# Kernel optimization log

Measured on AMD Instinct MI355X. Metric: run time of the kernel, lower is better.

The kernel has to match this reference:

```python
import jax, jax.numpy as jnp
import numpy as np
import math

PI = math.pi
PHI = (1.0 + math.sqrt(5.0)) / 2.0
D_MODEL = 1024
N_HEADS = 16
D_HEAD = D_MODEL // N_HEADS
LAYER_DEPTH = 0.5
LAYER_INDEX = 0
CONV_RATE = 0.1


def setup_inputs() -> dict:
    key = jax.random.key(0)
    ks = jax.random.split(key, 5)
    B, T = 2, 2048
    x = jax.random.normal(ks[0], (B, T, D_MODEL), dtype=jnp.float32)
    s = 1.0 / math.sqrt(D_MODEL)
    Wq = jax.random.normal(ks[1], (D_MODEL, D_MODEL), dtype=jnp.float32) * s
    Wk = jax.random.normal(ks[2], (D_MODEL, D_MODEL), dtype=jnp.float32) * s
    Wv = jax.random.normal(ks[3], (D_MODEL, D_MODEL), dtype=jnp.float32) * s
    We = jax.random.normal(ks[4], (D_MODEL, D_MODEL), dtype=jnp.float32) * s
    # per-head chamber init, matching ApertureChamber / _head_depth
    frac = jnp.arange(N_HEADS, dtype=jnp.float32) / max(N_HEADS - 1, 1)
    lo = LAYER_DEPTH * 0.5
    hi = 0.5 + LAYER_DEPTH * 0.5
    depth = lo + frac * (hi - lo)
    beta = 0.5 + 0.2 * (1.0 - 2.0 * depth)           # [H] raw (pre-sigmoid) params
    input_valve = jnp.full((N_HEADS,), 0.5, dtype=jnp.float32)
    output_valve = jnp.full((N_HEADS,), 0.5, dtype=jnp.float32)
    chi = jnp.ones((N_HEADS,), dtype=jnp.float32)
    return {"x": x, "Wq": Wq, "Wk": Wk, "Wv": Wv, "We": We,
            "beta": beta, "input_valve": input_valve,
            "output_valve": output_valve, "chi": chi}


def reference(x, Wq, Wk, Wv, We, beta, input_valve, output_valve, chi):
    B, T, D = x.shape
    H, dh = N_HEADS, D // N_HEADS
    conv_factor = 1.0 / PHI ** (LAYER_INDEX * CONV_RATE)
    scale = math.sqrt(dh * conv_factor)
    # QKV projections (torch Linear: x @ W.T), split heads -> [B,H,T,dh]
    q = (x @ Wq.T).reshape(B, T, H, dh).transpose(0, 2, 1, 3)
    k = (x @ Wk.T).reshape(B, T, H, dh).transpose(0, 2, 1, 3)
    v = (x @ Wv.T).reshape(B, T, H, dh).transpose(0, 2, 1, 3)
    attn = jax.nn.softmax(jnp.einsum('bhqd,bhkd->bhqk', q, k) / scale, axis=-1)
    converged = jnp.einsum('bhqk,bhkd->bhqd', attn, v)  # [B,H,T,dh]
    # ApertureChamber per head, vectorized over H (broadcast [H] -> [1,H,1,1])
    b = jax.nn.sigmoid(beta)[None, :, None, None]
    iv = jax.nn.sigmoid(input_valve)[None, :, None, None]
    ov = jax.nn.sigmoid(output_valve)[None, :, None, None]
    g = jnp.tanh(chi)[None, :, None, None]
    ang = PI * b
    ca, sa = jnp.cos(ang), jnp.sin(ang)
    x_in = converged * iv
    half = dh // 2  # d_head even -> no leftover lane
    xr, xi = x_in[..., :half], x_in[..., half:]
    rot = jnp.concatenate([xr * ca - xi * sa, xr * sa + xi * ca], axis=-1)
    out = rot * ov * g  # output valve + tanh(chi) gate
    combined = out.transpose(0, 2, 1, 3).reshape(B, T, D)
    return combined @ We.T
```

## Files before the change

kernel.cpp:

```cpp
#include <hip/hip_runtime.h>
#include <hip/hip_bf16.h>
#include <math.h>

typedef __bf16 bf16;
typedef __bf16 bf16x4 __attribute__((ext_vector_type(4)));
typedef __bf16 bf16x8 __attribute__((ext_vector_type(8)));
typedef float f32x4 __attribute__((ext_vector_type(4)));
typedef float f32x16 __attribute__((ext_vector_type(16)));
typedef unsigned int u32x4 __attribute__((ext_vector_type(4)));

static __device__ __forceinline__ f32x4 mfma16(bf16x8 a, bf16x8 b, f32x4 c) {
  return __builtin_amdgcn_mfma_f32_16x16x32_bf16(a, b, c, 0, 0, 0);
}
static __device__ __forceinline__ f32x16 mfma32(bf16x8 a, bf16x8 b, f32x16 c) {
  return __builtin_amdgcn_mfma_f32_32x32x16_bf16(a, b, c, 0, 0, 0);
}
static __device__ __forceinline__ void gld_lds16(const void* g, void* l) {
  __builtin_amdgcn_global_load_lds(
      (const __attribute__((address_space(1))) void*)g,
      (__attribute__((address_space(3))) void*)l, 16, 0, 0);
}
static __device__ __forceinline__ unsigned cvt_pk_bf16(float lo, float hi) {
  unsigned r;
  asm("v_cvt_pk_bf16_f32 %0, %1, %2" : "=v"(r) : "v"(lo), "v"(hi));
  return r;
}
static __device__ __forceinline__ float rsum16(f32x16 v) {
  float a0 = v[0] + v[8],  a1 = v[1] + v[9];
  float a2 = v[2] + v[10], a3 = v[3] + v[11];
  float a4 = v[4] + v[12], a5 = v[5] + v[13];
  float a6 = v[6] + v[14], a7 = v[7] + v[15];
  a0 += a4; a1 += a5; a2 += a6; a3 += a7;
  return (a0 + a1) + (a2 + a3);
}

__global__ void cast_all(const float* __restrict__ x, const float* __restrict__ Wq,
                         const float* __restrict__ Wk, const float* __restrict__ Wv,
                         const float* __restrict__ We,
                         bf16* __restrict__ xb, bf16* __restrict__ qb,
                         bf16* __restrict__ kb, bf16* __restrict__ vb,
                         bf16* __restrict__ eb) {
  int i = blockIdx.x * 256 + threadIdx.x;
  const float* s; bf16* d; int off;
  if (i < 1048576) { s = x; d = xb; off = i; }
  else {
    int j = i - 1048576; int w = j >> 18; off = j & 262143;
    s = (w == 0) ? Wq : (w == 1) ? Wk : (w == 2) ? Wv : We;
    d = (w == 0) ? qb : (w == 1) ? kb : (w == 2) ? vb : eb;
  }
  float4 v = reinterpret_cast<const float4*>(s)[off];
  bf16x4 o; o[0] = (bf16)v.x; o[1] = (bf16)v.y; o[2] = (bf16)v.z; o[3] = (bf16)v.w;
  reinterpret_cast<bf16x4*>(d)[off] = o;
}

template<int MODE>
__global__ void gemm_bt(const bf16* __restrict__ A,
                        const bf16* __restrict__ B0, const bf16* __restrict__ B1,
                        const bf16* __restrict__ B2,
                        void* __restrict__ C0v, void* __restrict__ C1v, void* __restrict__ C2v,
                        int M, int N, int K) {
  __shared__ bf16 As[128 * 64];
  __shared__ bf16 Bs[128 * 64];
  const int tid = threadIdx.x;
  const int wave = tid >> 6;
  const int lane = tid & 63;
  const int bid = blockIdx.x | (blockIdx.y << 3) | (blockIdx.z << 8);
  const int cpx = gridDim.z << 5;
  const int swz = (bid & 7) * cpx + (bid >> 3);
  const int n0 = (swz & 7) * 128;
  const int m0 = ((swz >> 3) & 31) * 128;
  const int zz = swz >> 8;
  const bf16* B = (zz == 0) ? B0 : (zz == 1) ? B1 : B2;
  void* Cv = (zz == 0) ? C0v : (zz == 1) ? C1v : C2v;
  const int wr = (wave >> 1) * 64;
  const int wc = (wave & 1) * 64;
  const int frow = lane & 15;
  const int fx = frow & 7;
  const int khi = lane >> 4;
  const int srow8 = lane >> 3;
  const int scol = ((lane & 7) ^ srow8) * 8;
  f32x4 acc[4][4] = {};
  char* AsB = (char*)As;
  char* BsB = (char*)Bs;
  for (int k0 = 0; k0 < K; k0 += 64) {
    __syncthreads();
#pragma unroll
    for (int j = 0; j < 4; ++j) {
      int u = j * 4 + wave;
      int row = u * 8 + srow8;
      gld_lds16(&A[(size_t)(m0 + row) * K + k0 + scol], AsB + u * 1024);
      gld_lds16(&B[(size_t)(n0 + row) * K + k0 + scol], BsB + u * 1024);
    }
    asm volatile("s_waitcnt vmcnt(0)" ::: "memory");
    __syncthreads();
#pragma unroll
    for (int kk = 0; kk < 2; ++kk) {
      bf16x8 af[4], bfr[4];
#pragma unroll
      for (int mi = 0; mi < 4; ++mi)
        af[mi] = *reinterpret_cast<const bf16x8*>(
            AsB + (wr + mi * 16 + frow) * 128 + (((kk << 2) + khi) ^ fx) * 16);
#pragma unroll
      for (int ni = 0; ni < 4; ++ni)
        bfr[ni] = *reinterpret_cast<const bf16x8*>(
            BsB + (wc + ni * 16 + frow) * 128 + (((kk << 2) + khi) ^ fx) * 16);
      __builtin_amdgcn_s_setprio(1);
#pragma unroll
      for (int mi = 0; mi < 4; ++mi)
#pragma unroll
        for (int ni = 0; ni < 4; ++ni)
          acc[mi][ni] = mfma16(af[mi], bfr[ni], acc[mi][ni]);
      __builtin_amdgcn_s_setprio(0);
    }
  }
#pragma unroll
  for (int mi = 0; mi < 4; ++mi) {
#pragma unroll
    for (int ni = 0; ni < 4; ++ni) {
#pragma unroll
      for (int r = 0; r < 4; ++r) {
        int row = m0 + wr + mi * 16 + khi * 4 + r;
        int col = n0 + wc + ni * 16 + frow;
        if (MODE == 0) {
          int b = row >> 11, t = row & 2047, h = col >> 6, d = col & 63;
          ((bf16*)Cv)[(((size_t)b * 16 + h) * 2048 + t) * 64 + d] = (bf16)acc[mi][ni][r];
        } else {
          ((float*)Cv)[(size_t)row * N + col] = acc[mi][ni][r];
        }
      }
    }
  }
}

__global__ void transpose_v(const bf16* __restrict__ v, bf16* __restrict__ vt) {
  __shared__ bf16 tile[64][65];
  int bh = blockIdx.y;
  int t0 = blockIdx.x * 64;
  for (int idx = threadIdx.x; idx < 64 * 64; idx += 256) {
    int r = idx >> 6, c = idx & 63;
    tile[r][c] = v[((size_t)bh * 2048 + t0 + r) * 64 + c];
  }
  __syncthreads();
  for (int idx = threadIdx.x; idx < 64 * 64; idx += 256) {
    int d = idx >> 6, r = idx & 63;
    vt[((size_t)bh * 64 + d) * 2048 + t0 + r] = tile[r][d];
  }
}

__global__ __launch_bounds__(256, 4)
void attn_kernel(const bf16* __restrict__ q, const bf16* __restrict__ k,
                 const bf16* __restrict__ vt,
                 const float* __restrict__ beta, const float* __restrict__ ivp,
                 const float* __restrict__ ovp, const float* __restrict__ chip,
                 bf16* __restrict__ comb) {
  __shared__ bf16 Ks[2][64 * 64];
  __shared__ bf16 Vs[2][64 * 64];
  const int tid = threadIdx.x;
  const int wave = tid >> 6, lane = tid & 63;
  const int hi = lane >> 5, ln = lane & 31;
  const int bid = blockIdx.x | (blockIdx.y << 4);
  const int swz = (bid & 7) * 64 + (bid >> 3);
  const int qblk = swz & 15, bh = swz >> 4;
  const int h = bh & 15, b = bh >> 4;
  const int q0w = qblk * 128 + wave * 32;
  const float C = 0.18033688011112042f;
  const float SHIFT = 28.853900817779268f;

  const bf16* qrow = q + ((size_t)bh * 2048 + q0w + ln) * 64 + hi * 8;
  bf16x8 qf[4];
#pragma unroll
  for (int ds = 0; ds < 4; ++ds)
    qf[ds] = *reinterpret_cast<const bf16x8*>(qrow + ds * 16);

  const bf16* kbase = k + (size_t)bh * 2048 * 64;
  const bf16* vbase = vt + (size_t)bh * 64 * 2048;
  const int srow = lane >> 3;
  const int scol = ((lane & 7) ^ (srow & 7)) * 8;

  f32x16 acc0 = {}, acc1 = {}, ps = {};

  auto stage = [&](int buf, int k0) {
#pragma unroll
    for (int j = 0; j < 2; ++j) {
      int u = wave * 2 + j;
      int r = u * 8 + srow;
      gld_lds16(&kbase[(size_t)(k0 + r) * 64 + scol], (char*)&Ks[buf][0] + u * 1024);
      gld_lds16(&vbase[(size_t)r * 2048 + k0 + scol], (char*)&Vs[buf][0] + u * 1024);
    }
  };

  stage(0, 0);
  int cur = 0;
  for (int k0 = 0; k0 < 2048; k0 += 64) {
    asm volatile("s_waitcnt vmcnt(0)" ::: "memory");
    __syncthreads();
    if (k0 + 64 < 2048) stage(cur ^ 1, k0 + 64);

    f32x16 s[2];
    s[0] = (f32x16){}; s[1] = (f32x16){};
    const char* kb = (const char*)&Ks[cur][0];
    __builtin_amdgcn_s_setprio(1);
#pragma unroll
    for (int kh = 0; kh < 2; ++kh) {
      const int r = kh * 32 + ln;
      const int rx = (r & 7) << 4;
#pragma unroll
      for (int ds = 0; ds < 4; ++ds) {
        bf16x8 kf = *reinterpret_cast<const bf16x8*>(kb + r * 128 + ((ds * 32 + hi * 16) ^ rx));
        s[kh] = mfma32(kf, qf[ds], s[kh]);
      }
    }
    __builtin_amdgcn_s_setprio(0);

#pragma unroll
    for (int kh = 0; kh < 2; ++kh) {
      f32x16 z = s[kh] * C - SHIFT;
#pragma unroll
      for (int e = 0; e < 16; ++e) s[kh][e] = exp2f(z[e]);
      ps += s[kh];
    }

    const char* vb = (const char*)&Vs[cur][0];
#pragma unroll
    for (int ks = 0; ks < 4; ++ks) {
      const int kh = ks >> 1;
      const int b0 = 8 * (ks & 1);
      unsigned a0 = cvt_pk_bf16(s[kh][b0 + 0], s[kh][b0 + 1]);
      unsigned a1 = cvt_pk_bf16(s[kh][b0 + 4], s[kh][b0 + 5]);
      unsigned c0 = cvt_pk_bf16(s[kh][b0 + 2], s[kh][b0 + 3]);
      unsigned c1 = cvt_pk_bf16(s[kh][b0 + 6], s[kh][b0 + 7]);
      asm("v_permlane32_swap_b32 %0, %1" : "+v"(a0), "+v"(a1));
      asm("v_permlane32_swap_b32 %0, %1" : "+v"(c0), "+v"(c1));
      union { u32x4 u; bf16x8 v; } pf;
      pf.u[0] = a0; pf.u[1] = c0; pf.u[2] = a1; pf.u[3] = c1;
      __builtin_amdgcn_s_setprio(1);
#pragma unroll
      for (int dh = 0; dh < 2; ++dh) {
        const int r = dh * 32 + ln;
        bf16x8 vf = *reinterpret_cast<const bf16x8*>(
            vb + r * 128 + ((ks * 32 + hi * 16) ^ ((r & 7) << 4)));
        if (dh == 0) acc0 = mfma32(pf.v, vf, acc0);
        else         acc1 = mfma32(pf.v, vf, acc1);
      }
      __builtin_amdgcn_s_setprio(0);
    }
    cur ^= 1;
  }

  float lsum = rsum16(ps);
  lsum += __shfl_xor(lsum, 32);
  float inv = 1.f / lsum;

  float bb = 1.f / (1.f + expf(-beta[h]));
  float ang = 3.14159265358979323846f * bb;
  float ca = cosf(ang), sa = sinf(ang);
  float iv = 1.f / (1.f + expf(-ivp[h]));
  float ov = 1.f / (1.f + expf(-ovp[h]));
  float g = tanhf(chip[h]);
  float K1 = iv * ov * g * ca;
  float K2 = iv * ov * g * sa;
#pragma unroll
  for (int r = 0; r < 16; ++r) {
    int qr = (r & 3) + 8 * (r >> 2) + 4 * hi;
    float iq = __shfl(inv, qr, 32);
    float o_r = acc0[r] * iq, o_i = acc1[r] * iq;
    size_t base = ((size_t)b * 2048 + q0w + qr) * 1024 + (size_t)h * 64;
    comb[base + ln]      = (bf16)(K1 * o_r - K2 * o_i);
    comb[base + 32 + ln] = (bf16)(K2 * o_r + K1 * o_i);
  }
}

extern "C" void kernel_launch(void* const* d_in, const int* in_sizes, int n_in,
                              void* d_out, int out_size, void* d_ws, size_t ws_size,
                              hipStream_t stream) {
  const float* x    = (const float*)d_in[0];
  const float* Wq   = (const float*)d_in[1];
  const float* Wk   = (const float*)d_in[2];
  const float* Wv   = (const float*)d_in[3];
  const float* We   = (const float*)d_in[4];
  const float* beta = (const float*)d_in[5];
  const float* ivp  = (const float*)d_in[6];
  const float* ovp  = (const float*)d_in[7];
  const float* chip = (const float*)d_in[8];

  char* ws = (char*)d_ws;
  bf16* x_bf  = (bf16*)(ws + (size_t)0);
  bf16* Wq_bf = (bf16*)(ws + ((size_t)8  << 20));
  bf16* Wk_bf = (bf16*)(ws + ((size_t)10 << 20));
  bf16* Wv_bf = (bf16*)(ws + ((size_t)12 << 20));
  bf16* We_bf = (bf16*)(ws + ((size_t)14 << 20));
  bf16* q_bf  = (bf16*)(ws + ((size_t)16 << 20));
  bf16* k_bf  = (bf16*)(ws + ((size_t)24 << 20));
  bf16* v_bf  = (bf16*)(ws + ((size_t)32 << 20));
  bf16* v_t   = (bf16*)(ws + ((size_t)40 << 20));
  bf16* comb  = (bf16*)(ws + ((size_t)48 << 20));

  cast_all<<<8192, 256, 0, stream>>>(x, Wq, Wk, Wv, We, x_bf, Wq_bf, Wk_bf, Wv_bf, We_bf);

  gemm_bt<0><<<dim3(8, 32, 3), 256, 0, stream>>>(x_bf, Wq_bf, Wk_bf, Wv_bf,
                                                 q_bf, k_bf, v_bf, 4096, 1024, 1024);
  transpose_v<<<dim3(32, 32), 256, 0, stream>>>(v_bf, v_t);
  attn_kernel<<<dim3(16, 32), 256, 0, stream>>>(q_bf, k_bf, v_t, beta, ivp, ovp, chip, comb);
  gemm_bt<1><<<dim3(8, 32, 1), 256, 0, stream>>>(comb, We_bf, We_bf, We_bf,
                                                 d_out, d_out, d_out, 4096, 1024, 1024);
}
```

Baseline: 226.8 us.

## Split attention KV range across two wave groups and merge partial sums in LDS

Doubles the attention block to 512 threads, where two groups of four waves each process half of the key/value sequence for the same 128 queries, with separate double-buffered LDS tiles. After the loop, group 1 writes its unnormalized accumulators and row sums to LDS and group 0 adds them before normalizing and applying the rotation gate. The goal is more waves in flight per query tile to hide latency and shorten the per-block serial loop. The cost is double the LDS per block (64KB), a cross-group reduction through shared memory, and possibly lower occupancy. The fixed softmax shift keeps the merge a plain sum.

```diff
diff --git a/kernel.cpp b/kernel.cpp
--- a/kernel.cpp
+++ b/kernel.cpp
@@ -147,22 +147,23 @@
   }
 }
 
-__global__ __launch_bounds__(256, 4)
+__global__ __launch_bounds__(512, 4)
 void attn_kernel(const bf16* __restrict__ q, const bf16* __restrict__ k,
                  const bf16* __restrict__ vt,
                  const float* __restrict__ beta, const float* __restrict__ ivp,
                  const float* __restrict__ ovp, const float* __restrict__ chip,
                  bf16* __restrict__ comb) {
-  __shared__ bf16 Ks[2][64 * 64];
-  __shared__ bf16 Vs[2][64 * 64];
+  __shared__ bf16 Ks[2][2][64 * 64];
+  __shared__ bf16 Vs[2][2][64 * 64];
   const int tid = threadIdx.x;
   const int wave = tid >> 6, lane = tid & 63;
+  const int w4 = wave & 3, grp = wave >> 2;
   const int hi = lane >> 5, ln = lane & 31;
   const int bid = blockIdx.x | (blockIdx.y << 4);
   const int swz = (bid & 7) * 64 + (bid >> 3);
   const int qblk = swz & 15, bh = swz >> 4;
   const int h = bh & 15, b = bh >> 4;
-  const int q0w = qblk * 128 + wave * 32;
+  const int q0w = qblk * 128 + w4 * 32;
   const float C = 0.18033688011112042f;
   const float SHIFT = 28.853900817779268f;
 
@@ -172,33 +173,34 @@
   for (int ds = 0; ds < 4; ++ds)
     qf[ds] = *reinterpret_cast<const bf16x8*>(qrow + ds * 16);
 
-  const bf16* kbase = k + (size_t)bh * 2048 * 64;
-  const bf16* vbase = vt + (size_t)bh * 64 * 2048;
+  const bf16* kbase = k + (size_t)bh * 2048 * 64 + (size_t)grp * 1024 * 64;
+  const bf16* vbase = vt + (size_t)bh * 64 * 2048 + grp * 1024;
   const int srow = lane >> 3;
   const int scol = ((lane & 7) ^ (srow & 7)) * 8;
 
-  f32x16 acc0 = {}, acc1 = {}, ps = {};
+  f32x16 acc0 = {}, acc1 = {};
+  float lsum = 0.f;
 
   auto stage = [&](int buf, int k0) {
 #pragma unroll
     for (int j = 0; j < 2; ++j) {
-      int u = wave * 2 + j;
+      int u = w4 * 2 + j;
       int r = u * 8 + srow;
-      gld_lds16(&kbase[(size_t)(k0 + r) * 64 + scol], (char*)&Ks[buf][0] + u * 1024);
-      gld_lds16(&vbase[(size_t)r * 2048 + k0 + scol], (char*)&Vs[buf][0] + u * 1024);
+      gld_lds16(&kbase[(size_t)(k0 + r) * 64 + scol], (char*)&Ks[grp][buf][0] + u * 1024);
+      gld_lds16(&vbase[(size_t)r * 2048 + k0 + scol], (char*)&Vs[grp][buf][0] + u * 1024);
     }
   };
 
   stage(0, 0);
   int cur = 0;
-  for (int k0 = 0; k0 < 2048; k0 += 64) {
+  for (int k0 = 0; k0 < 1024; k0 += 64) {
     asm volatile("s_waitcnt vmcnt(0)" ::: "memory");
     __syncthreads();
-    if (k0 + 64 < 2048) stage(cur ^ 1, k0 + 64);
+    if (k0 + 64 < 1024) stage(cur ^ 1, k0 + 64);
 
     f32x16 s[2];
     s[0] = (f32x16){}; s[1] = (f32x16){};
-    const char* kb = (const char*)&Ks[cur][0];
+    const char* kb = (const char*)&Ks[grp][cur][0];
     __builtin_amdgcn_s_setprio(1);
 #pragma unroll
     for (int kh = 0; kh < 2; ++kh) {
@@ -217,10 +219,10 @@
       f32x16 z = s[kh] * C - SHIFT;
 #pragma unroll
       for (int e = 0; e < 16; ++e) s[kh][e] = exp2f(z[e]);
-      ps += s[kh];
-    }
-
-    const char* vb = (const char*)&Vs[cur][0];
+      lsum += rsum16(s[kh]);
+    }
+
+    const char* vb = (const char*)&Vs[grp][cur][0];
 #pragma unroll
     for (int ks = 0; ks < 4; ++ks) {
       const int kh = ks >> 1;
@@ -247,26 +249,46 @@
     cur ^= 1;
   }
 
-  float lsum = rsum16(ps);
-  lsum += __shfl_xor(lsum, 32);
-  float inv = 1.f / lsum;
-
-  float bb = 1.f / (1.f + expf(-beta[h]));
-  float ang = 3.14159265358979323846f * bb;
-  float ca = cosf(ang), sa = sinf(ang);
-  float iv = 1.f / (1.f + expf(-ivp[h]));
-  float ov = 1.f / (1.f + expf(-ovp[h]));
-  float g = tanhf(chip[h]);
-  float K1 = iv * ov * g * ca;
-  float K2 = iv * ov * g * sa;
-#pragma unroll
-  for (int r = 0; r < 16; ++r) {
-    int qr = (r & 3) + 8 * (r >> 2) + 4 * hi;
-    float iq = __shfl(inv, qr, 32);
-    float o_r = acc0[r] * iq, o_i = acc1[r] * iq;
-    size_t base = ((size_t)b * 2048 + q0w + qr) * 1024 + (size_t)h * 64;
-    comb[base + ln]      = (bf16)(K1 * o_r - K2 * o_i);
-    comb[base + 32 + ln] = (bf16)(K2 * o_r + K1 * o_i);
+  __syncthreads();
+  float* exO = (float*)&Ks[0][0][0];
+  float* exL = (float*)&Vs[0][0][0];
+  const int xl = w4 * 64 + lane;
+  if (grp == 1) {
+#pragma unroll
+    for (int r = 0; r < 16; ++r) {
+      exO[r * 256 + xl]        = acc0[r];
+      exO[(16 + r) * 256 + xl] = acc1[r];
+    }
+    exL[xl] = lsum;
+  }
+  __syncthreads();
+  if (grp == 0) {
+#pragma unroll
+    for (int r = 0; r < 16; ++r) {
+      acc0[r] += exO[r * 256 + xl];
+      acc1[r] += exO[(16 + r) * 256 + xl];
+    }
+    lsum += exL[xl];
+    lsum += __shfl_xor(lsum, 32);
+    float inv = 1.f / lsum;
+
+    float bb = 1.f / (1.f + expf(-beta[h]));
+    float ang = 3.14159265358979323846f * bb;
+    float ca = cosf(ang), sa = sinf(ang);
+    float iv = 1.f / (1.f + expf(-ivp[h]));
+    float ov = 1.f / (1.f + expf(-ovp[h]));
+    float g = tanhf(chip[h]);
+    float K1 = iv * ov * g * ca;
+    float K2 = iv * ov * g * sa;
+#pragma unroll
+    for (int r = 0; r < 16; ++r) {
+      int qr = (r & 3) + 8 * (r >> 2) + 4 * hi;
+      float iq = __shfl(inv, qr, 32);
+      float o_r = acc0[r] * iq, o_i = acc1[r] * iq;
+      size_t base = ((size_t)b * 2048 + q0w + qr) * 1024 + (size_t)h * 64;
+      comb[base + ln]      = (bf16)(K1 * o_r - K2 * o_i);
+      comb[base + 32 + ln] = (bf16)(K2 * o_r + K1 * o_i);
+    }
   }
 }
 
@@ -300,7 +322,7 @@
   gemm_bt<0><<<dim3(8, 32, 3), 256, 0, stream>>>(x_bf, Wq_bf, Wk_bf, Wv_bf,
                                                  q_bf, k_bf, v_bf, 4096, 1024, 1024);
   transpose_v<<<dim3(32, 32), 256, 0, stream>>>(v_bf, v_t);
-  attn_kernel<<<dim3(16, 32), 256, 0, stream>>>(q_bf, k_bf, v_t, beta, ivp, ovp, chip, comb);
+  attn_kernel<<<dim3(16, 32), 512, 0, stream>>>(q_bf, k_bf, v_t, beta, ivp, ovp, chip, comb);
   gemm_bt<1><<<dim3(8, 32, 1), 256, 0, stream>>>(comb, We_bf, We_bf, We_bf,
                                                  d_out, d_out, d_out, 4096, 1024, 1024);
 }
```

Result: faster. 203.3 us (-10.4%).
